# Performance work log

Hardware: AMD Instinct MI355X
Metric: run time of the kernel (lower is better)

Reference implementation:

```python
import jax, jax.numpy as jnp
import numpy as np

N_NODES = 100000
N_EDGES = 800000
N_GRAPHS = 128
BN_EPS = 1e-5


def _bn(h, g, b, m, v):
    # BatchNorm1d in eval mode: uses running stats
    return (h - m) * jax.lax.rsqrt(v + BN_EPS) * g + b


def _gin_layer(x, edge_index, eps, wa, ba, g, be, m, v, wb, bb):
    src, dst = edge_index[0], edge_index[1]
    # sparse neighbor sum: scatter-add messages x[src] into dst
    agg = jax.ops.segment_sum(x[src], dst, num_segments=N_NODES)
    h = (1.0 + eps) * x + agg  # eps shape [1] broadcasts
    h = jax.nn.relu(_bn(h @ wa + ba, g, be, m, v))
    return jax.nn.relu(h @ wb + bb)


def setup_inputs() -> dict:
    key = jax.random.key(0)
    ks = jax.random.split(key, 12)
    inp = {
        'x': jax.random.normal(ks[0], (N_NODES, 384), dtype=jnp.float32),
        'edge_index': jax.random.randint(ks[1], (2, N_EDGES), 0, N_NODES, dtype=jnp.int64),
        'batch': jnp.sort(jax.random.randint(ks[2], (N_NODES,), 0, N_GRAPHS, dtype=jnp.int64)),
        'eps1': jnp.zeros((1,), jnp.float32),
        'w1a': jax.random.normal(ks[3], (384, 128), jnp.float32) * 0.05,
        'b1a': jnp.zeros((128,), jnp.float32),
        'g1': jnp.ones((128,), jnp.float32), 'be1': jnp.zeros((128,), jnp.float32),
        'm1': jnp.zeros((128,), jnp.float32), 'v1': jnp.ones((128,), jnp.float32),
        'w1b': jax.random.normal(ks[4], (128, 128), jnp.float32) * 0.05,
        'b1b': jnp.zeros((128,), jnp.float32),
        'eps2': jnp.zeros((1,), jnp.float32),
        'w2a': jax.random.normal(ks[5], (128, 128), jnp.float32) * 0.05,
        'b2a': jnp.zeros((128,), jnp.float32),
        'g2': jnp.ones((128,), jnp.float32), 'be2': jnp.zeros((128,), jnp.float32),
        'm2': jnp.zeros((128,), jnp.float32), 'v2': jnp.ones((128,), jnp.float32),
        'w2b': jax.random.normal(ks[6], (128, 128), jnp.float32) * 0.05,
        'b2b': jnp.zeros((128,), jnp.float32),
        'eps3': jnp.zeros((1,), jnp.float32),
        'w3a': jax.random.normal(ks[7], (128, 128), jnp.float32) * 0.05,
        'b3a': jnp.zeros((128,), jnp.float32),
        'g3': jnp.ones((128,), jnp.float32), 'be3': jnp.zeros((128,), jnp.float32),
        'm3': jnp.zeros((128,), jnp.float32), 'v3': jnp.ones((128,), jnp.float32),
        'w3b': jax.random.normal(ks[8], (128, 64), jnp.float32) * 0.05,
        'b3b': jnp.zeros((64,), jnp.float32),
        'wc': jax.random.normal(ks[9], (64, 2), jnp.float32) * 0.05,
        'bc': jnp.zeros((2,), jnp.float32),
    }
    return inp


def reference(x, edge_index, batch,
              eps1, w1a, b1a, g1, be1, m1, v1, w1b, b1b,
              eps2, w2a, b2a, g2, be2, m2, v2, w2b, b2b,
              eps3, w3a, b3a, g3, be3, m3, v3, w3b, b3b,
              wc, bc):
    h = _gin_layer(x, edge_index, eps1, w1a, b1a, g1, be1, m1, v1, w1b, b1b)
    # dropout is identity in eval mode
    h = _gin_layer(h, edge_index, eps2, w2a, b2a, g2, be2, m2, v2, w2b, b2b)
    h = _gin_layer(h, edge_index, eps3, w3a, b3a, g3, be3, m3, v3, w3b, b3b)
    # global add pool over graphs
    pooled = jax.ops.segment_sum(h, batch, num_segments=N_GRAPHS)  # [G, 64]
    return pooled @ wc + bc  # [G, num_classes]
```

## Files before the change

kernel.cpp:

```cpp
#include <hip/hip_runtime.h>
#include <hip/hip_bf16.h>


#define N_NODES 100000
#define N_EDGES 800000
#define N_GRAPHS 128
#define NB_SCAN 391
#define LDP 136
#define FLDP 68
#define G1_BLOCKS 1563
#define HIST_BLOCKS 782

typedef __bf16 bf16x8 __attribute__((ext_vector_type(8)));
typedef float f32x4 __attribute__((ext_vector_type(4)));
typedef unsigned short ushort_t;
typedef unsigned int uint_t;

static __device__ __forceinline__ ushort_t f2b(float f) {
    uint_t u = __builtin_bit_cast(uint_t, f);
    uint_t r = (u + 0x7fffu + ((u >> 16) & 1u)) >> 16;
    return (ushort_t)r;
}
static __device__ __forceinline__ float b2f(ushort_t u) {
    return __builtin_bit_cast(float, (uint_t)u << 16);
}

__global__ __launch_bounds__(256) void wt_all_k(
        const float* __restrict__ w1a, const float* __restrict__ w1b,
        const float* __restrict__ w2a, const float* __restrict__ w2b,
        const float* __restrict__ w3a, const float* __restrict__ w3b,
        ushort_t* __restrict__ o1a, ushort_t* __restrict__ o1b,
        ushort_t* __restrict__ o2a, ushort_t* __restrict__ o2b,
        ushort_t* __restrict__ o3a, ushort_t* __restrict__ o3b,
        int* __restrict__ ideg, float* __restrict__ pooled) {
    int t = blockIdx.x * 256 + threadIdx.x;
    if (t < 122880) {
        const float* W; ushort_t* O; int K, N, i;
        if      (t <  49152) { W = w1a; O = o1a; K = 384; N = 128; i = t; }
        else if (t <  65536) { W = w1b; O = o1b; K = 128; N = 128; i = t - 49152; }
        else if (t <  81920) { W = w2a; O = o2a; K = 128; N = 128; i = t - 65536; }
        else if (t <  98304) { W = w2b; O = o2b; K = 128; N = 128; i = t - 81920; }
        else if (t < 114688) { W = w3a; O = o3a; K = 128; N = 128; i = t - 98304; }
        else                 { W = w3b; O = o3b; K = 128; N = 64;  i = t - 114688; }
        int k = i / N, c = i % N;
        O[c * K + k] = f2b(W[i]);
    } else if (t < 222880) {
        ideg[t - 122880] = 0;
    } else if (t < 231072) {
        pooled[t - 222880] = 0.f;
    }
}

__global__ __launch_bounds__(256) void gemm1_hist_k(const float* __restrict__ A,
                                                    const ushort_t* __restrict__ Wt,
                                                    ushort_t* __restrict__ C, int M,
                                                    const int* __restrict__ dst,
                                                    int* __restrict__ deg) {
    __shared__ ushort_t Al[64 * LDP];

    if (blockIdx.x >= G1_BLOCKS) {
        int b = blockIdx.x - G1_BLOCKS;
        int e0 = b * 1024 + threadIdx.x;
        #pragma unroll
        for (int p = 0; p < 4; ++p) {
            int e = e0 + p * 256;
            if (e < N_EDGES) atomicAdd(&deg[dst[e]], 1);
        }
        return;
    }

    constexpr int K = 384;
    const int tid  = threadIdx.x;
    const int lane = tid & 63;
    const int wid  = tid >> 6;
    const int wrow = wid >> 1;
    const int wcol = wid & 1;
    const int l15  = lane & 15;
    const int kg   = lane >> 4;
    const int row0 = blockIdx.x * 64;

    f32x4 acc[2][4];
    #pragma unroll
    for (int i = 0; i < 2; ++i)
        #pragma unroll
        for (int j = 0; j < 4; ++j)
            acc[i][j] = f32x4{0.f, 0.f, 0.f, 0.f};

    const int r  = tid >> 2;
    const int cc = (tid & 3) * 32;

    for (int k0 = 0; k0 < K; k0 += 128) {
        __syncthreads();
        {
            int gr = row0 + r;
            if (gr > M - 1) gr = M - 1;
            const float* pA = A + (size_t)gr * K + k0 + cc;
            float4 v[8];
            #pragma unroll
            for (int p = 0; p < 8; ++p)
                v[p] = *reinterpret_cast<const float4*>(pA + p * 4);
            uint_t u[16];
            #pragma unroll
            for (int p = 0; p < 8; ++p) {
                u[2 * p]     = (uint_t)f2b(v[p].x) | ((uint_t)f2b(v[p].y) << 16);
                u[2 * p + 1] = (uint_t)f2b(v[p].z) | ((uint_t)f2b(v[p].w) << 16);
            }
            uint4* dstp = reinterpret_cast<uint4*>(&Al[r * LDP + cc]);
            dstp[0] = make_uint4(u[0], u[1], u[2], u[3]);
            dstp[1] = make_uint4(u[4], u[5], u[6], u[7]);
            dstp[2] = make_uint4(u[8], u[9], u[10], u[11]);
            dstp[3] = make_uint4(u[12], u[13], u[14], u[15]);
        }
        __syncthreads();

        #pragma unroll
        for (int kk = 0; kk < 4; ++kk) {
            bf16x8 a0 = *reinterpret_cast<const bf16x8*>(&Al[(wrow * 32 + l15) * LDP + kk * 32 + kg * 8]);
            bf16x8 a1 = *reinterpret_cast<const bf16x8*>(&Al[(wrow * 32 + 16 + l15) * LDP + kk * 32 + kg * 8]);
            #pragma unroll
            for (int j = 0; j < 4; ++j) {
                int col = wcol * 64 + j * 16 + l15;
                bf16x8 b = *reinterpret_cast<const bf16x8*>(Wt + (size_t)col * K + k0 + kk * 32 + kg * 8);
                acc[0][j] = __builtin_amdgcn_mfma_f32_16x16x32_bf16(a0, b, acc[0][j], 0, 0, 0);
                acc[1][j] = __builtin_amdgcn_mfma_f32_16x16x32_bf16(a1, b, acc[1][j], 0, 0, 0);
            }
        }
    }

    __syncthreads();
    #pragma unroll
    for (int i = 0; i < 2; ++i)
        #pragma unroll
        for (int j = 0; j < 4; ++j) {
            int col = wcol * 64 + j * 16 + l15;
            #pragma unroll
            for (int q = 0; q < 4; ++q) {
                int row = wrow * 32 + i * 16 + kg * 4 + q;
                Al[row * LDP + col] = f2b(acc[i][j][q]);
            }
        }
    __syncthreads();
    #pragma unroll
    for (int p = 0; p < 4; ++p) {
        int idx = tid + p * 256;
        int rr = idx >> 4, c16 = idx & 15;
        int gr = row0 + rr;
        if (gr < M)
            *reinterpret_cast<uint4*>(C + (size_t)gr * 128 + c16 * 8) =
                *reinterpret_cast<const uint4*>(&Al[rr * LDP + c16 * 8]);
    }
}

__global__ __launch_bounds__(256) void scan1_k(const int* __restrict__ deg,
                                               int* __restrict__ tmp,
                                               int* __restrict__ bsum) {
    __shared__ int s[256];
    int i = blockIdx.x * 256 + threadIdx.x;
    int t = threadIdx.x;
    s[t] = (i < N_NODES) ? deg[i] : 0;
    __syncthreads();
    for (int off = 1; off < 256; off <<= 1) {
        int v = (t >= off) ? s[t - off] : 0;
        __syncthreads();
        s[t] += v;
        __syncthreads();
    }
    if (i < N_NODES) tmp[i] = s[t];
    if (t == 255) bsum[blockIdx.x] = s[255];
}

__global__ __launch_bounds__(256) void scan23_k(const int* __restrict__ tmp,
                                                const int* __restrict__ deg,
                                                const int* __restrict__ bsum,
                                                int* __restrict__ row_start) {
    __shared__ int sb[256];
    int t = threadIdx.x;
    int partial = 0;
    for (int i = t; i < (int)blockIdx.x; i += 256) partial += bsum[i];
    sb[t] = partial;
    __syncthreads();
    for (int off = 128; off > 0; off >>= 1) {
        if (t < off) sb[t] += sb[t + off];
        __syncthreads();
    }
    int boff = sb[0];
    int i = blockIdx.x * 256 + t;
    if (i < N_NODES) row_start[i] = tmp[i] - deg[i] + boff;
}

__global__ __launch_bounds__(256) void fill_k(const int* __restrict__ src,
                                              const int* __restrict__ dst,
                                              int* __restrict__ row_start,
                                              int* __restrict__ csr_src) {
    int e = blockIdx.x * 256 + threadIdx.x;
    if (e >= N_EDGES) return;
    int idx = atomicAdd(&row_start[dst[e]], 1);
    csr_src[idx] = src[e];
}

__global__ __launch_bounds__(256) void gather_bn_k(
        const ushort_t* __restrict__ Yin,
        const int* __restrict__ csr, const int* __restrict__ rend,
        const int* __restrict__ deg,
        const float* __restrict__ epsp, const float* __restrict__ ba,
        const float* __restrict__ g, const float* __restrict__ be,
        const float* __restrict__ mm, const float* __restrict__ vv,
        ushort_t* __restrict__ H, int nwaves) {
    const int gwid = (blockIdx.x * 256 + threadIdx.x) >> 6;
    const int lane = threadIdx.x & 63;
    const int l15  = lane & 15;
    const int slot = lane >> 4;
    const int c0   = l15 * 8;

    float ep = 1.0f + epsp[0];
    float sc[8], sh[8];
    #pragma unroll
    for (int jj = 0; jj < 8; ++jj) {
        int c = c0 + jj;
        float s = g[c] * rsqrtf(vv[c] + 1e-5f);
        sc[jj] = s;
        sh[jj] = (ba[c] - mm[c]) * s + be[c];
    }

    int node = gwid;
    if (node >= N_NODES) return;
    int end = rend[node], d = deg[node];
    int st = end - d;
    int nlim = (d > 64) ? 64 : d;
    int nb = (lane < nlim) ? csr[st + lane] : 0;

    for (; node < N_NODES; node += nwaves) {
        const int nnode = node + nwaves;
        int nend = 0, nd = 0;
        if (nnode < N_NODES) { nend = rend[nnode]; nd = deg[nnode]; }

        uint4 ow = *reinterpret_cast<const uint4*>(Yin + (size_t)node * 128 + c0);

        float acc[8] = {0.f, 0.f, 0.f, 0.f, 0.f, 0.f, 0.f, 0.f};
        for (int j0 = 0; j0 < nlim; j0 += 8) {
            int jA = j0 + slot;
            int jB = j0 + 4 + slot;
            int ia = __shfl(nb, jA & 63);
            int ib = __shfl(nb, jB & 63);
            uint4 wa = *reinterpret_cast<const uint4*>(Yin + (size_t)ia * 128 + c0);
            uint4 wb = *reinterpret_cast<const uint4*>(Yin + (size_t)ib * 128 + c0);
            float fa = (jA < nlim) ? 1.f : 0.f;
            float fb = (jB < nlim) ? 1.f : 0.f;
            uint_t ua[4] = {wa.x, wa.y, wa.z, wa.w};
            uint_t ub[4] = {wb.x, wb.y, wb.z, wb.w};
            #pragma unroll
            for (int p = 0; p < 4; ++p) {
                acc[2 * p]     += fa * b2f((ushort_t)(ua[p] & 0xffff));
                acc[2 * p + 1] += fa * b2f((ushort_t)(ua[p] >> 16));
                acc[2 * p]     += fb * b2f((ushort_t)(ub[p] & 0xffff));
                acc[2 * p + 1] += fb * b2f((ushort_t)(ub[p] >> 16));
            }
        }
        for (int j = st + 64; j < end; ++j) {
            if (slot == 0) {
                int idx = csr[j];
                uint4 w = *reinterpret_cast<const uint4*>(Yin + (size_t)idx * 128 + c0);
                uint_t uw[4] = {w.x, w.y, w.z, w.w};
                #pragma unroll
                for (int p = 0; p < 4; ++p) {
                    acc[2 * p]     += b2f((ushort_t)(uw[p] & 0xffff));
                    acc[2 * p + 1] += b2f((ushort_t)(uw[p] >> 16));
                }
            }
        }

        int nst = nend - nd;
        int nnlim = (nd > 64) ? 64 : nd;
        int nb2 = 0;
        if (nnode < N_NODES && lane < nnlim) nb2 = csr[nst + lane];

        #pragma unroll
        for (int jj = 0; jj < 8; ++jj) {
            acc[jj] += __shfl_xor(acc[jj], 16);
            acc[jj] += __shfl_xor(acc[jj], 32);
        }
        uint_t uo[4] = {ow.x, ow.y, ow.z, ow.w};
        ushort_t rr[8];
        #pragma unroll
        for (int p = 0; p < 4; ++p) {
            float o0 = b2f((ushort_t)(uo[p] & 0xffff));
            float o1 = b2f((ushort_t)(uo[p] >> 16));
            float t0 = sc[2 * p] * (ep * o0 + acc[2 * p]) + sh[2 * p];
            float t1 = sc[2 * p + 1] * (ep * o1 + acc[2 * p + 1]) + sh[2 * p + 1];
            rr[2 * p]     = f2b(fmaxf(t0, 0.f));
            rr[2 * p + 1] = f2b(fmaxf(t1, 0.f));
        }
        if (slot == 0) {
            uint4 packed;
            packed.x = (uint_t)rr[0] | ((uint_t)rr[1] << 16);
            packed.y = (uint_t)rr[2] | ((uint_t)rr[3] << 16);
            packed.z = (uint_t)rr[4] | ((uint_t)rr[5] << 16);
            packed.w = (uint_t)rr[6] | ((uint_t)rr[7] << 16);
            *reinterpret_cast<uint4*>(H + (size_t)node * 128 + c0) = packed;
        }

        end = nend; d = nd; st = nst; nlim = nnlim; nb = nb2;
    }
}

template<bool TAIL>
__global__ __launch_bounds__(256) void mlp_k(const ushort_t* __restrict__ Hin,
                                             const ushort_t* __restrict__ Wb,
                                             const float* __restrict__ bias1,
                                             const ushort_t* __restrict__ Wa2,
                                             ushort_t* __restrict__ Yout,
                                             const int* __restrict__ batch,
                                             float* __restrict__ pooled, int M) {
    constexpr int BM = 64;
    constexpr int NJ1 = TAIL ? 2 : 4;
    __shared__ ushort_t Hl[BM * LDP];
    __shared__ ushort_t Xl[BM * LDP];
    float* Fl = (float*)Xl;

    const int tid  = threadIdx.x;
    const int lane = tid & 63;
    const int wid  = tid >> 6;
    const int wrow = wid >> 1;
    const int wcol = wid & 1;
    const int l15  = lane & 15;
    const int kg   = lane >> 4;
    const int row0 = blockIdx.x * BM;

    #pragma unroll
    for (int p = 0; p < 4; ++p) {
        int idx = tid + p * 256;
        int r = idx >> 4, c16 = idx & 15;
        int gr = row0 + r;
        if (gr > M - 1) gr = M - 1;
        *reinterpret_cast<uint4*>(&Hl[r * LDP + c16 * 8]) =
            *reinterpret_cast<const uint4*>(Hin + (size_t)gr * 128 + c16 * 8);
    }
    __syncthreads();

    f32x4 acc1[2][NJ1];
    #pragma unroll
    for (int i = 0; i < 2; ++i)
        #pragma unroll
        for (int j = 0; j < NJ1; ++j)
            acc1[i][j] = f32x4{0.f, 0.f, 0.f, 0.f};
    #pragma unroll
    for (int kk = 0; kk < 4; ++kk) {
        bf16x8 a0 = *reinterpret_cast<const bf16x8*>(&Hl[(wrow * 32 + l15) * LDP + kk * 32 + kg * 8]);
        bf16x8 a1 = *reinterpret_cast<const bf16x8*>(&Hl[(wrow * 32 + 16 + l15) * LDP + kk * 32 + kg * 8]);
        #pragma unroll
        for (int j = 0; j < NJ1; ++j) {
            int col = wcol * (16 * NJ1) + j * 16 + l15;
            bf16x8 b = *reinterpret_cast<const bf16x8*>(Wb + (size_t)col * 128 + kk * 32 + kg * 8);
            acc1[0][j] = __builtin_amdgcn_mfma_f32_16x16x32_bf16(a0, b, acc1[0][j], 0, 0, 0);
            acc1[1][j] = __builtin_amdgcn_mfma_f32_16x16x32_bf16(a1, b, acc1[1][j], 0, 0, 0);
        }
    }

    if constexpr (TAIL) {
        #pragma unroll
        for (int i = 0; i < 2; ++i)
            #pragma unroll
            for (int j = 0; j < NJ1; ++j) {
                int col = wcol * 32 + j * 16 + l15;
                float bi = bias1[col];
                #pragma unroll
                for (int q = 0; q < 4; ++q) {
                    int row = wrow * 32 + i * 16 + kg * 4 + q;
                    Fl[row * FLDP + col] = fmaxf(acc1[i][j][q] + bi, 0.f);
                }
            }
        __syncthreads();
        int col = tid & 63;
        int qq  = tid >> 6;
        float a = 0.f;
        int cur = -1;
        for (int rr = 0; rr < 16; ++rr) {
            int r = qq * 16 + rr;
            int gr = row0 + r;
            if (gr >= M) break;
            int b = batch[gr];
            if (b != cur) {
                if (cur >= 0) atomicAdd(&pooled[cur * 64 + col], a);
                a = 0.f;
                cur = b;
            }
            a += Fl[r * FLDP + col];
        }
        if (cur >= 0) atomicAdd(&pooled[cur * 64 + col], a);
    } else {
        #pragma unroll
        for (int i = 0; i < 2; ++i)
            #pragma unroll
            for (int j = 0; j < NJ1; ++j) {
                int col = wcol * 64 + j * 16 + l15;
                float bi = bias1[col];
                #pragma unroll
                for (int q = 0; q < 4; ++q) {
                    int row = wrow * 32 + i * 16 + kg * 4 + q;
                    Xl[row * LDP + col] = f2b(fmaxf(acc1[i][j][q] + bi, 0.f));
                }
            }
        __syncthreads();

        f32x4 acc2[2][4];
        #pragma unroll
        for (int i = 0; i < 2; ++i)
            #pragma unroll
            for (int j = 0; j < 4; ++j)
                acc2[i][j] = f32x4{0.f, 0.f, 0.f, 0.f};
        #pragma unroll
        for (int kk = 0; kk < 4; ++kk) {
            bf16x8 a0 = *reinterpret_cast<const bf16x8*>(&Xl[(wrow * 32 + l15) * LDP + kk * 32 + kg * 8]);
            bf16x8 a1 = *reinterpret_cast<const bf16x8*>(&Xl[(wrow * 32 + 16 + l15) * LDP + kk * 32 + kg * 8]);
            #pragma unroll
            for (int j = 0; j < 4; ++j) {
                int col = wcol * 64 + j * 16 + l15;
                bf16x8 b = *reinterpret_cast<const bf16x8*>(Wa2 + (size_t)col * 128 + kk * 32 + kg * 8);
                acc2[0][j] = __builtin_amdgcn_mfma_f32_16x16x32_bf16(a0, b, acc2[0][j], 0, 0, 0);
                acc2[1][j] = __builtin_amdgcn_mfma_f32_16x16x32_bf16(a1, b, acc2[1][j], 0, 0, 0);
            }
        }
        #pragma unroll
        for (int i = 0; i < 2; ++i)
            #pragma unroll
            for (int j = 0; j < 4; ++j) {
                int col = wcol * 64 + j * 16 + l15;
                #pragma unroll
                for (int q = 0; q < 4; ++q) {
                    int row = wrow * 32 + i * 16 + kg * 4 + q;
                    Hl[row * LDP + col] = f2b(acc2[i][j][q]);
                }
            }
        __syncthreads();
        #pragma unroll
        for (int p = 0; p < 4; ++p) {
            int idx = tid + p * 256;
            int r = idx >> 4, c16 = idx & 15;
            int gr = row0 + r;
            if (gr < M)
                *reinterpret_cast<uint4*>(Yout + (size_t)gr * 128 + c16 * 8) =
                    *reinterpret_cast<const uint4*>(&Hl[r * LDP + c16 * 8]);
        }
    }
}

__global__ __launch_bounds__(256) void classifier_k(const float* __restrict__ pooled,
                                                    const float* __restrict__ wc,
                                                    const float* __restrict__ bc,
                                                    float* __restrict__ out) {
    int t = threadIdx.x;
    int gidx = t >> 1, c = t & 1;
    float s = bc[c];
    #pragma unroll
    for (int k = 0; k < 64; ++k)
        s += pooled[gidx * 64 + k] * wc[k * 2 + c];
    out[gidx * 2 + c] = s;
}

extern "C" void kernel_launch(void* const* d_in, const int* in_sizes, int n_in,
                              void* d_out, int out_size, void* d_ws, size_t ws_size,
                              hipStream_t stream) {
    const float* x     = (const float*)d_in[0];
    const int*   ei    = (const int*)d_in[1];
    const int*   src   = ei;
    const int*   dst   = ei + N_EDGES;
    const int*   batch = (const int*)d_in[2];
    const float* eps1 = (const float*)d_in[3];
    const float* w1a  = (const float*)d_in[4];
    const float* b1a  = (const float*)d_in[5];
    const float* g1   = (const float*)d_in[6];
    const float* be1  = (const float*)d_in[7];
    const float* m1   = (const float*)d_in[8];
    const float* v1   = (const float*)d_in[9];
    const float* w1b  = (const float*)d_in[10];
    const float* b1b  = (const float*)d_in[11];
    const float* eps2 = (const float*)d_in[12];
    const float* w2a  = (const float*)d_in[13];
    const float* b2a  = (const float*)d_in[14];
    const float* g2   = (const float*)d_in[15];
    const float* be2  = (const float*)d_in[16];
    const float* m2   = (const float*)d_in[17];
    const float* v2   = (const float*)d_in[18];
    const float* w2b  = (const float*)d_in[19];
    const float* b2b  = (const float*)d_in[20];
    const float* eps3 = (const float*)d_in[21];
    const float* w3a  = (const float*)d_in[22];
    const float* b3a  = (const float*)d_in[23];
    const float* g3   = (const float*)d_in[24];
    const float* be3  = (const float*)d_in[25];
    const float* m3   = (const float*)d_in[26];
    const float* v3   = (const float*)d_in[27];
    const float* w3b  = (const float*)d_in[28];
    const float* b3b  = (const float*)d_in[29];
    const float* wc   = (const float*)d_in[30];
    const float* bc   = (const float*)d_in[31];
    float* out = (float*)d_out;

    ushort_t* Y = (ushort_t*)d_ws;
    ushort_t* H = Y + 12800000;
    ushort_t* wt1a = H + 12800000;
    ushort_t* wt1b = wt1a + 49152;
    ushort_t* wt2a = wt1b + 16384;
    ushort_t* wt2b = wt2a + 16384;
    ushort_t* wt3a = wt2b + 16384;
    ushort_t* wt3b = wt3a + 16384;
    float* pooled = (float*)(wt3b + 8192);
    int* ideg = (int*)(pooled + 8192);
    int* irow = ideg + N_NODES;
    int* itmp = irow + N_NODES;
    int* icsr = itmp + N_NODES;
    int* ibsum = icsr + N_EDGES;

    const int M = N_NODES;
    const int gGemm = (M + 63) / 64;
    const int gEdge = (N_EDGES + 255) / 256;
    const int gNode = NB_SCAN;
    const int gGath = 2048;
    const int nwaves = gGath * 4;

    wt_all_k<<<903, 256, 0, stream>>>(w1a, w1b, w2a, w2b, w3a, w3b,
                                      wt1a, wt1b, wt2a, wt2b, wt3a, wt3b,
                                      ideg, pooled);

    gemm1_hist_k<<<G1_BLOCKS + HIST_BLOCKS, 256, 0, stream>>>(x, wt1a, Y, M, dst, ideg);

    scan1_k<<<gNode, 256, 0, stream>>>(ideg, itmp, ibsum);
    scan23_k<<<gNode, 256, 0, stream>>>(itmp, ideg, ibsum, irow);
    fill_k<<<gEdge, 256, 0, stream>>>(src, dst, irow, icsr);

    gather_bn_k<<<gGath, 256, 0, stream>>>(Y, icsr, irow, ideg, eps1, b1a, g1, be1, m1, v1, H, nwaves);
    mlp_k<false><<<gGemm, 256, 0, stream>>>(H, wt1b, b1b, wt2a, Y, nullptr, nullptr, M);

    gather_bn_k<<<gGath, 256, 0, stream>>>(Y, icsr, irow, ideg, eps2, b2a, g2, be2, m2, v2, H, nwaves);
    mlp_k<false><<<gGemm, 256, 0, stream>>>(H, wt2b, b2b, wt3a, Y, nullptr, nullptr, M);

    gather_bn_k<<<gGath, 256, 0, stream>>>(Y, icsr, irow, ideg, eps3, b3a, g3, be3, m3, v3, H, nwaves);
    mlp_k<true><<<gGemm, 256, 0, stream>>>(H, wt3b, b3b, nullptr, nullptr, batch, pooled, M);

    classifier_k<<<1, 256, 0, stream>>>(pooled, wc, bc, out);
}
```

Baseline: 373.0 us.

## Fuse neighbor gather+BN into the per-tile MLP kernel, ping-pong Y/H buffers

Merges the gather/BatchNorm kernel into the MLP GEMM kernel. Each 64-row block now gathers its own nodes into shared memory (16 nodes per wave) and then runs the two matmuls directly, with no round trip through the H buffer in global memory. Layers alternate between the Y and H buffers so a layer never overwrites its own input, and a barrier is added before shared memory is reused. The cost is that the gather loses its grid-stride structure and load balancing (1563 blocks, fixed 16 nodes per wave), and the shared-memory footprint may limit occupancy during the gather phase.

```diff
diff --git a/kernel.cpp b/kernel.cpp
--- a/kernel.cpp
+++ b/kernel.cpp
@@ -198,144 +198,128 @@
     csr_src[idx] = src[e];
 }
 
-__global__ __launch_bounds__(256) void gather_bn_k(
+template<bool TAIL>
+__global__ __launch_bounds__(256) void gather_mlp_k(
         const ushort_t* __restrict__ Yin,
         const int* __restrict__ csr, const int* __restrict__ rend,
         const int* __restrict__ deg,
         const float* __restrict__ epsp, const float* __restrict__ ba,
         const float* __restrict__ g, const float* __restrict__ be,
         const float* __restrict__ mm, const float* __restrict__ vv,
-        ushort_t* __restrict__ H, int nwaves) {
-    const int gwid = (blockIdx.x * 256 + threadIdx.x) >> 6;
-    const int lane = threadIdx.x & 63;
+        const ushort_t* __restrict__ Wb, const float* __restrict__ bias1,
+        const ushort_t* __restrict__ Wa2,
+        ushort_t* __restrict__ Yout,
+        const int* __restrict__ batch, float* __restrict__ pooled, int M) {
+    constexpr int NJ1 = TAIL ? 2 : 4;
+    __shared__ ushort_t Hl[64 * LDP];
+    __shared__ ushort_t Xl[64 * LDP];
+    float* Fl = (float*)Xl;
+
+    const int tid  = threadIdx.x;
+    const int lane = tid & 63;
+    const int wid  = tid >> 6;
     const int l15  = lane & 15;
     const int slot = lane >> 4;
     const int c0   = l15 * 8;
-
-    float ep = 1.0f + epsp[0];
-    float sc[8], sh[8];
-    #pragma unroll
-    for (int jj = 0; jj < 8; ++jj) {
-        int c = c0 + jj;
-        float s = g[c] * rsqrtf(vv[c] + 1e-5f);
-        sc[jj] = s;
-        sh[jj] = (ba[c] - mm[c]) * s + be[c];
-    }
-
-    int node = gwid;
-    if (node >= N_NODES) return;
-    int end = rend[node], d = deg[node];
-    int st = end - d;
-    int nlim = (d > 64) ? 64 : d;
-    int nb = (lane < nlim) ? csr[st + lane] : 0;
-
-    for (; node < N_NODES; node += nwaves) {
-        const int nnode = node + nwaves;
-        int nend = 0, nd = 0;
-        if (nnode < N_NODES) { nend = rend[nnode]; nd = deg[nnode]; }
-
-        uint4 ow = *reinterpret_cast<const uint4*>(Yin + (size_t)node * 128 + c0);
-
-        float acc[8] = {0.f, 0.f, 0.f, 0.f, 0.f, 0.f, 0.f, 0.f};
-        for (int j0 = 0; j0 < nlim; j0 += 8) {
-            int jA = j0 + slot;
-            int jB = j0 + 4 + slot;
-            int ia = __shfl(nb, jA & 63);
-            int ib = __shfl(nb, jB & 63);
-            uint4 wa = *reinterpret_cast<const uint4*>(Yin + (size_t)ia * 128 + c0);
-            uint4 wb = *reinterpret_cast<const uint4*>(Yin + (size_t)ib * 128 + c0);
-            float fa = (jA < nlim) ? 1.f : 0.f;
-            float fb = (jB < nlim) ? 1.f : 0.f;
-            uint_t ua[4] = {wa.x, wa.y, wa.z, wa.w};
-            uint_t ub[4] = {wb.x, wb.y, wb.z, wb.w};
-            #pragma unroll
-            for (int p = 0; p < 4; ++p) {
-                acc[2 * p]     += fa * b2f((ushort_t)(ua[p] & 0xffff));
-                acc[2 * p + 1] += fa * b2f((ushort_t)(ua[p] >> 16));
-                acc[2 * p]     += fb * b2f((ushort_t)(ub[p] & 0xffff));
-                acc[2 * p + 1] += fb * b2f((ushort_t)(ub[p] >> 16));
-            }
-        }
-        for (int j = st + 64; j < end; ++j) {
-            if (slot == 0) {
-                int idx = csr[j];
-                uint4 w = *reinterpret_cast<const uint4*>(Yin + (size_t)idx * 128 + c0);
-                uint_t uw[4] = {w.x, w.y, w.z, w.w};
+    const int row0 = blockIdx.x * 64;
+
+    {
+        float ep = 1.0f + epsp[0];
+        float sc[8], sh[8];
+        #pragma unroll
+        for (int jj = 0; jj < 8; ++jj) {
+            int c = c0 + jj;
+            float s = g[c] * rsqrtf(vv[c] + 1e-5f);
+            sc[jj] = s;
+            sh[jj] = (ba[c] - mm[c]) * s + be[c];
+        }
+
+        const int base = row0 + wid * 16;
+        int cn = base; if (cn > M - 1) cn = M - 1;
+        int end = rend[cn], d = deg[cn];
+        int st = end - d;
+        int nlim = (d > 64) ? 64 : d;
+        int nb = (lane < nlim) ? csr[st + lane] : 0;
+
+        for (int nl = 0; nl < 16; ++nl) {
+            int node = base + nl; if (node > M - 1) node = M - 1;
+            int nxt = base + nl + 1; if (nxt > M - 1) nxt = M - 1;
+            int nend = 0, nd = 0;
+            if (nl < 15) { nend = rend[nxt]; nd = deg[nxt]; }
+
+            uint4 ow = *reinterpret_cast<const uint4*>(Yin + (size_t)node * 128 + c0);
+
+            float acc[8] = {0.f, 0.f, 0.f, 0.f, 0.f, 0.f, 0.f, 0.f};
+            for (int j0 = 0; j0 < nlim; j0 += 8) {
+                int jA = j0 + slot;
+                int jB = j0 + 4 + slot;
+                int ia = __shfl(nb, jA & 63);
+                int ib = __shfl(nb, jB & 63);
+                uint4 wa = *reinterpret_cast<const uint4*>(Yin + (size_t)ia * 128 + c0);
+                uint4 wb = *reinterpret_cast<const uint4*>(Yin + (size_t)ib * 128 + c0);
+                float fa = (jA < nlim) ? 1.f : 0.f;
+                float fb = (jB < nlim) ? 1.f : 0.f;
+                uint_t ua[4] = {wa.x, wa.y, wa.z, wa.w};
+                uint_t ub[4] = {wb.x, wb.y, wb.z, wb.w};
                 #pragma unroll
                 for (int p = 0; p < 4; ++p) {
-                    acc[2 * p]     += b2f((ushort_t)(uw[p] & 0xffff));
-                    acc[2 * p + 1] += b2f((ushort_t)(uw[p] >> 16));
+                    acc[2 * p]     += fa * b2f((ushort_t)(ua[p] & 0xffff));
+                    acc[2 * p + 1] += fa * b2f((ushort_t)(ua[p] >> 16));
+                    acc[2 * p]     += fb * b2f((ushort_t)(ub[p] & 0xffff));
+                    acc[2 * p + 1] += fb * b2f((ushort_t)(ub[p] >> 16));
                 }
             }
-        }
-
-        int nst = nend - nd;
-        int nnlim = (nd > 64) ? 64 : nd;
-        int nb2 = 0;
-        if (nnode < N_NODES && lane < nnlim) nb2 = csr[nst + lane];
-
-        #pragma unroll
-        for (int jj = 0; jj < 8; ++jj) {
-            acc[jj] += __shfl_xor(acc[jj], 16);
-            acc[jj] += __shfl_xor(acc[jj], 32);
-        }
-        uint_t uo[4] = {ow.x, ow.y, ow.z, ow.w};
-        ushort_t rr[8];
-        #pragma unroll
-        for (int p = 0; p < 4; ++p) {
-            float o0 = b2f((ushort_t)(uo[p] & 0xffff));
-            float o1 = b2f((ushort_t)(uo[p] >> 16));
-            float t0 = sc[2 * p] * (ep * o0 + acc[2 * p]) + sh[2 * p];
-            float t1 = sc[2 * p + 1] * (ep * o1 + acc[2 * p + 1]) + sh[2 * p + 1];
-            rr[2 * p]     = f2b(fmaxf(t0, 0.f));
-            rr[2 * p + 1] = f2b(fmaxf(t1, 0.f));
-        }
-        if (slot == 0) {
-            uint4 packed;
-            packed.x = (uint_t)rr[0] | ((uint_t)rr[1] << 16);
-            packed.y = (uint_t)rr[2] | ((uint_t)rr[3] << 16);
-            packed.z = (uint_t)rr[4] | ((uint_t)rr[5] << 16);
-            packed.w = (uint_t)rr[6] | ((uint_t)rr[7] << 16);
-            *reinterpret_cast<uint4*>(H + (size_t)node * 128 + c0) = packed;
-        }
-
-        end = nend; d = nd; st = nst; nlim = nnlim; nb = nb2;
-    }
-}
-
-template<bool TAIL>
-__global__ __launch_bounds__(256) void mlp_k(const ushort_t* __restrict__ Hin,
-                                             const ushort_t* __restrict__ Wb,
-                                             const float* __restrict__ bias1,
-                                             const ushort_t* __restrict__ Wa2,
-                                             ushort_t* __restrict__ Yout,
-                                             const int* __restrict__ batch,
-                                             float* __restrict__ pooled, int M) {
-    constexpr int BM = 64;
-    constexpr int NJ1 = TAIL ? 2 : 4;
-    __shared__ ushort_t Hl[BM * LDP];
-    __shared__ ushort_t Xl[BM * LDP];
-    float* Fl = (float*)Xl;
-
-    const int tid  = threadIdx.x;
-    const int lane = tid & 63;
-    const int wid  = tid >> 6;
+            for (int j = st + 64; j < end; ++j) {
+                if (slot == 0) {
+                    int idx = csr[j];
+                    uint4 w = *reinterpret_cast<const uint4*>(Yin + (size_t)idx * 128 + c0);
+                    uint_t uw[4] = {w.x, w.y, w.z, w.w};
+                    #pragma unroll
+                    for (int p = 0; p < 4; ++p) {
+                        acc[2 * p]     += b2f((ushort_t)(uw[p] & 0xffff));
+                        acc[2 * p + 1] += b2f((ushort_t)(uw[p] >> 16));
+                    }
+                }
+            }
+
+            int nst = nend - nd;
+            int nnlim = (nd > 64) ? 64 : nd;
+            int nb2 = 0;
+            if (nl < 15 && lane < nnlim) nb2 = csr[nst + lane];
+
+            #pragma unroll
+            for (int jj = 0; jj < 8; ++jj) {
+                acc[jj] += __shfl_xor(acc[jj], 16);
+                acc[jj] += __shfl_xor(acc[jj], 32);
+            }
+            uint_t uo[4] = {ow.x, ow.y, ow.z, ow.w};
+            ushort_t rr[8];
+            #pragma unroll
+            for (int p = 0; p < 4; ++p) {
+                float o0 = b2f((ushort_t)(uo[p] & 0xffff));
+                float o1 = b2f((ushort_t)(uo[p] >> 16));
+                float t0 = sc[2 * p] * (ep * o0 + acc[2 * p]) + sh[2 * p];
+                float t1 = sc[2 * p + 1] * (ep * o1 + acc[2 * p + 1]) + sh[2 * p + 1];
+                rr[2 * p]     = f2b(fmaxf(t0, 0.f));
+                rr[2 * p + 1] = f2b(fmaxf(t1, 0.f));
+            }
+            if (slot == 0) {
+                uint4 packed;
+                packed.x = (uint_t)rr[0] | ((uint_t)rr[1] << 16);
+                packed.y = (uint_t)rr[2] | ((uint_t)rr[3] << 16);
+                packed.z = (uint_t)rr[4] | ((uint_t)rr[5] << 16);
+                packed.w = (uint_t)rr[6] | ((uint_t)rr[7] << 16);
+                *reinterpret_cast<uint4*>(&Hl[(wid * 16 + nl) * LDP + c0]) = packed;
+            }
+
+            end = nend; d = nd; st = nst; nlim = nnlim; nb = nb2;
+        }
+    }
+    __syncthreads();
+
     const int wrow = wid >> 1;
     const int wcol = wid & 1;
-    const int l15  = lane & 15;
     const int kg   = lane >> 4;
-    const int row0 = blockIdx.x * BM;
-
-    #pragma unroll
-    for (int p = 0; p < 4; ++p) {
-        int idx = tid + p * 256;
-        int r = idx >> 4, c16 = idx & 15;
-        int gr = row0 + r;
-        if (gr > M - 1) gr = M - 1;
-        *reinterpret_cast<uint4*>(&Hl[r * LDP + c16 * 8]) =
-            *reinterpret_cast<const uint4*>(Hin + (size_t)gr * 128 + c16 * 8);
-    }
-    __syncthreads();
 
     f32x4 acc1[2][NJ1];
     #pragma unroll
@@ -374,8 +358,8 @@
         int qq  = tid >> 6;
         float a = 0.f;
         int cur = -1;
-        for (int rr = 0; rr < 16; ++rr) {
-            int r = qq * 16 + rr;
+        for (int rr2 = 0; rr2 < 16; ++rr2) {
+            int r = qq * 16 + rr2;
             int gr = row0 + r;
             if (gr >= M) break;
             int b = batch[gr];
@@ -420,6 +404,7 @@
                 acc2[1][j] = __builtin_amdgcn_mfma_f32_16x16x32_bf16(a1, b, acc2[1][j], 0, 0, 0);
             }
         }
+        __syncthreads();
         #pragma unroll
         for (int i = 0; i < 2; ++i)
             #pragma unroll
@@ -515,8 +500,6 @@
     const int gGemm = (M + 63) / 64;
     const int gEdge = (N_EDGES + 255) / 256;
     const int gNode = NB_SCAN;
-    const int gGath = 2048;
-    const int nwaves = gGath * 4;
 
     wt_all_k<<<903, 256, 0, stream>>>(w1a, w1b, w2a, w2b, w3a, w3b,
                                       wt1a, wt1b, wt2a, wt2b, wt3a, wt3b,
@@ -528,14 +511,15 @@
     scan23_k<<<gNode, 256, 0, stream>>>(itmp, ideg, ibsum, irow);
     fill_k<<<gEdge, 256, 0, stream>>>(src, dst, irow, icsr);
 
-    gather_bn_k<<<gGath, 256, 0, stream>>>(Y, icsr, irow, ideg, eps1, b1a, g1, be1, m1, v1, H, nwaves);
-    mlp_k<false><<<gGemm, 256, 0, stream>>>(H, wt1b, b1b, wt2a, Y, nullptr, nullptr, M);
-
-    gather_bn_k<<<gGath, 256, 0, stream>>>(Y, icsr, irow, ideg, eps2, b2a, g2, be2, m2, v2, H, nwaves);
-    mlp_k<false><<<gGemm, 256, 0, stream>>>(H, wt2b, b2b, wt3a, Y, nullptr, nullptr, M);
-
-    gather_bn_k<<<gGath, 256, 0, stream>>>(Y, icsr, irow, ideg, eps3, b3a, g3, be3, m3, v3, H, nwaves);
-    mlp_k<true><<<gGemm, 256, 0, stream>>>(H, wt3b, b3b, nullptr, nullptr, batch, pooled, M);
+    gather_mlp_k<false><<<gGemm, 256, 0, stream>>>(
+        Y, icsr, irow, ideg, eps1, b1a, g1, be1, m1, v1,
+        wt1b, b1b, wt2a, H, nullptr, nullptr, M);
+    gather_mlp_k<false><<<gGemm, 256, 0, stream>>>(
+        H, icsr, irow, ideg, eps2, b2a, g2, be2, m2, v2,
+        wt2b, b2b, wt3a, Y, nullptr, nullptr, M);
+    gather_mlp_k<true><<<gGemm, 256, 0, stream>>>(
+        Y, icsr, irow, ideg, eps3, b3a, g3, be3, m3, v3,
+        wt3b, b3b, nullptr, nullptr, batch, pooled, M);
 
     classifier_k<<<1, 256, 0, stream>>>(pooled, wc, bc, out);
 }
```

After: 359.1 us. 1.04x faster.
